# Kernel tuning notes

Hardware: AMD Instinct MI355X
Metric: run time of the kernel (lower is better)

Reference implementation:

```python
import jax, jax.numpy as jnp
import numpy as np

N = 100000
E = 1600000
IN_C = 128
HEADS = 4
HEAD_D = 32  # out_channels(128) // heads(4)


def setup_inputs() -> dict:
    key = jax.random.key(0)
    k1, k2, k3, k4, k5, k6 = jax.random.split(key, 6)
    x = jax.random.normal(k1, (N, IN_C), dtype=jnp.float32)
    edge_index = jax.random.randint(k2, (2, E), 0, N, dtype=jnp.int64)
    edge_weight = jax.random.uniform(k3, (E,), dtype=jnp.float32)
    # params: linear weight stored as [in, H*D] so forward is x @ W (torch does x @ weight.T)
    W = jax.random.normal(k4, (IN_C, HEADS * HEAD_D), dtype=jnp.float32) * (1.0 / np.sqrt(IN_C))
    att_src = jax.random.normal(k5, (HEADS, HEAD_D), dtype=jnp.float32) * 0.1
    att_dst = jax.random.normal(k6, (HEADS, HEAD_D), dtype=jnp.float32) * 0.1
    return {"x": x, "W": W, "att_src": att_src, "att_dst": att_dst,
            "edge_weight": edge_weight, "edge_index": edge_index, "num_nodes": N}


def reference(x, W, att_src, att_dst, edge_weight, edge_index, num_nodes):
    H, D = att_src.shape
    xw = (x @ W).reshape(-1, H, D)                       # [N, H, D]
    row, col = edge_index[0], edge_index[1]
    a_src = jnp.einsum('nhd,hd->nh', xw, att_src)        # [N, H]
    a_dst = jnp.einsum('nhd,hd->nh', xw, att_dst)        # [N, H]
    alpha = jax.nn.leaky_relu(a_src[row] + a_dst[col], negative_slope=0.2)  # [E, H]
    # segment softmax over edges grouped by row (destination of aggregation)
    amax = jax.ops.segment_max(alpha, row, num_segments=num_nodes)          # [N, H]
    amax = jnp.where(jnp.isfinite(amax), amax, 0.0)      # empty segments -> 0 (matches torch init)
    alpha = jnp.exp(alpha - amax[row])
    asum = jax.ops.segment_sum(alpha, row, num_segments=num_nodes)          # [N, H]
    alpha = alpha / (asum[row] + 1e-16)
    msg = xw[col] * alpha[..., None]                     # [E, H, D]
    out = jax.ops.segment_sum(msg, row, num_segments=num_nodes)             # [N, H, D]
    return out.reshape(num_nodes, H * D)
```

## Files before the change

kernel.cpp:

```cpp
#include <hip/hip_runtime.h>
#include <math.h>


typedef _Float16 half4 __attribute__((ext_vector_type(4)));
typedef _Float16 half8 __attribute__((ext_vector_type(8)));
typedef float    f32x4 __attribute__((ext_vector_type(4)));

#define PCHUNK   4096
#define NB_SHIFT 8
#define BCAP     4864

__device__ __forceinline__ float lrelu_exp(float v) {
    return __expf(fmaxf(v, 0.2f * v));
}

__global__ __launch_bounds__(128) void k_prep(const float* __restrict__ W,
                                              const float* __restrict__ att_src,
                                              const float* __restrict__ att_dst,
                                              _Float16* __restrict__ Wa) {
    int n = blockIdx.x;
    int k = threadIdx.x;
    float v;
    if (n < 128) {
        v = W[(size_t)k * 128 + n];
    } else if (n < 136) {
        int h = (n - 128) & 3;
        const float* att = (n < 132) ? att_src : att_dst;
        float s = 0.f;
        #pragma unroll
        for (int d = 0; d < 32; ++d)
            s += W[(size_t)k * 128 + h * 32 + d] * att[h * 32 + d];
        v = s;
    } else {
        v = 0.f;
    }
    Wa[n * 128 + k] = (_Float16)v;
}

__device__ __forceinline__ _Float16* lds_ptr(_Float16* base, int r, int kf16) {
    int g = (kf16 >> 3) ^ (r & 7);
    return base + r * 128 + g * 8 + (kf16 & 7);
}

__global__ __launch_bounds__(256) void k_gemm(const float* __restrict__ x,
                                              const _Float16* __restrict__ Wa,
                                              _Float16* __restrict__ xwh,
                                              float* __restrict__ a_src,
                                              float* __restrict__ a_dst, int N) {
    __shared__ _Float16 Xs[64 * 128];
    __shared__ _Float16 Ws[144 * 128];
    int t = threadIdx.x;
    int lane = t & 63, wv = t >> 6;
    int lm = lane & 15, lg = lane >> 4;
    int row0 = blockIdx.x * 64;

    #pragma unroll
    for (int i = 0; i < 9; ++i) {
        int f = (i * 256 + t) * 8;
        int nr = f >> 7, kc = f & 127;
        *(half8*)lds_ptr(Ws, nr, kc) = *(const half8*)&Wa[f];
    }
    #pragma unroll
    for (int i = 0; i < 4; ++i) {
        int f = (i * 256 + t) * 8;
        int r = f >> 7, kc = f & 127;
        int gr = row0 + r; if (gr >= N) gr = N - 1;
        float4 v0 = *(const float4*)&x[(size_t)gr * 128 + kc];
        float4 v1 = *(const float4*)&x[(size_t)gr * 128 + kc + 4];
        half8 hv;
        hv[0] = (_Float16)v0.x; hv[1] = (_Float16)v0.y;
        hv[2] = (_Float16)v0.z; hv[3] = (_Float16)v0.w;
        hv[4] = (_Float16)v1.x; hv[5] = (_Float16)v1.y;
        hv[6] = (_Float16)v1.z; hv[7] = (_Float16)v1.w;
        *(half8*)lds_ptr(Xs, r, kc) = hv;
    }
    __syncthreads();

    f32x4 acc[9];
    #pragma unroll
    for (int nn = 0; nn < 9; ++nn) acc[nn] = (f32x4){0.f, 0.f, 0.f, 0.f};

    #pragma unroll
    for (int kk = 0; kk < 4; ++kk) {
        int kb = kk * 32 + lg * 8;
        half8 a0 = *(const half8*)lds_ptr(Xs, wv * 16 + lm, kb);
        #pragma unroll
        for (int nn = 0; nn < 9; ++nn) {
            half8 b = *(const half8*)lds_ptr(Ws, nn * 16 + lm, kb);
            acc[nn] = __builtin_amdgcn_mfma_f32_16x16x32_f16(a0, b, acc[nn], 0, 0, 0);
        }
    }

    #pragma unroll
    for (int reg = 0; reg < 4; ++reg) {
        int row = row0 + wv * 16 + lg * 4 + reg;
        if (row < N) {
            #pragma unroll
            for (int nn = 0; nn < 8; ++nn)
                xwh[(size_t)row * 128 + nn * 16 + lm] = (_Float16)acc[nn][reg];
            float lv = acc[8][reg];
            if (lm < 4)      a_src[(size_t)row * 4 + lm]       = lv;
            else if (lm < 8) a_dst[(size_t)row * 4 + (lm - 4)] = lv;
        }
    }
}

__global__ __launch_bounds__(256) void k_part(const int* __restrict__ eidx,
                                              int* __restrict__ bctr,
                                              unsigned* __restrict__ rec,
                                              int E) {
    __shared__ unsigned long long buf[PCHUNK];
    __shared__ unsigned sbuf[PCHUNK];
    __shared__ int hist[512], excl[512], gbase[512], cur[512];
    __shared__ int wtot[4];
    int t = threadIdx.x;
    int lane = t & 63, wv = t >> 6;
    int e0 = blockIdx.x * PCHUNK;
    int nE = E - e0; if (nE > PCHUNK) nE = PCHUNK;
    hist[t] = 0; hist[t + 256] = 0;
    __syncthreads();
    for (int i = t; i < nE; i += 256) {
        int row = __builtin_nontemporal_load(&eidx[e0 + i]);
        int col = __builtin_nontemporal_load(&eidx[E + e0 + i]);
        buf[i] = ((unsigned long long)(unsigned)col << 32) | (unsigned)row;
        atomicAdd(&hist[row >> NB_SHIFT], 1);
    }
    __syncthreads();
    int h0 = hist[2 * t], h1 = hist[2 * t + 1];
    int s = h0 + h1, sc = s;
    #pragma unroll
    for (int off = 1; off < 64; off <<= 1) {
        int v = __shfl_up(sc, off);
        if (lane >= off) sc += v;
    }
    if (lane == 63) wtot[wv] = sc;
    __syncthreads();
    if (t == 0) {
        int run = 0;
        #pragma unroll
        for (int i = 0; i < 4; ++i) { int tmp = wtot[i]; wtot[i] = run; run += tmp; }
    }
    __syncthreads();
    int incl = sc + wtot[wv];
    excl[2 * t]     = incl - s;
    excl[2 * t + 1] = incl - h1;
    cur[2 * t]      = incl - s;
    cur[2 * t + 1]  = incl - h1;
    gbase[2 * t]     = h0 ? atomicAdd(&bctr[2 * t], h0) : 0;
    gbase[2 * t + 1] = h1 ? atomicAdd(&bctr[2 * t + 1], h1) : 0;
    __syncthreads();
    for (int i = t; i < nE; i += 256) {
        unsigned long long r = buf[i];
        int row = (int)(unsigned)r;
        int dst = atomicAdd(&cur[row >> NB_SHIFT], 1);
        sbuf[dst] = ((unsigned)(r >> 32) << 8) | ((unsigned)row & 255u);
    }
    __syncthreads();
    for (int j = t; j < nE; j += 256) {
        unsigned r = sbuf[j];
        int lo = 0;
        #pragma unroll
        for (int stp = 256; stp >= 1; stp >>= 1)
            if (lo + stp <= 511 && excl[lo + stp] <= j) lo += stp;
        int b = lo;
        int off = gbase[b] + (j - excl[b]);
        if (off < BCAP)
            __builtin_nontemporal_store(r, &rec[(size_t)b * BCAP + off]);
    }
}

__global__ __launch_bounds__(256) void k_csr(const unsigned* __restrict__ rec,
                                             const int* __restrict__ bctr,
                                             int2* __restrict__ rseg,
                                             int* __restrict__ csr_col, int N) {
    __shared__ int cnt[256], cur[256];
    __shared__ int wtot[4];
    int b = blockIdx.x;
    int rs = b << NB_SHIFT;
    int t = threadIdx.x;
    int lane = t & 63, wv = t >> 6;
    cnt[t] = 0;
    __syncthreads();
    int m = bctr[b]; if (m > BCAP) m = BCAP;
    const unsigned* rr = &rec[(size_t)b * BCAP];
    for (int i = t; i < m; i += 256) {
        unsigned r = rr[i];
        atomicAdd(&cnt[r & 255u], 1);
    }
    __syncthreads();
    int c = cnt[t], sc = c;
    #pragma unroll
    for (int off = 1; off < 64; off <<= 1) {
        int v = __shfl_up(sc, off);
        if (lane >= off) sc += v;
    }
    if (lane == 63) wtot[wv] = sc;
    __syncthreads();
    if (t == 0) {
        int run = 0;
        #pragma unroll
        for (int i = 0; i < 4; ++i) { int tmp = wtot[i]; wtot[i] = run; run += tmp; }
    }
    __syncthreads();
    int ex = sc + wtot[wv] - c;
    cur[t] = ex;
    int n = rs + t;
    if (n < N) {
        int2 sg;
        sg.x = b * BCAP + ex;
        sg.y = b * BCAP + ex + c;
        rseg[n] = sg;
    }
    __syncthreads();
    for (int i = t; i < m; i += 256) {
        unsigned r = rr[i];
        int slot = atomicAdd(&cur[r & 255u], 1);
        csr_col[b * BCAP + slot] = (int)(r >> 8);
    }
}

__global__ __launch_bounds__(256) void k_agg(const int2* __restrict__ rseg,
                                             const int* __restrict__ csr_col,
                                             const float* __restrict__ a_src,
                                             const float* __restrict__ a_dst,
                                             const _Float16* __restrict__ xwh,
                                             float* __restrict__ out, int N) {
    int lane = threadIdx.x & 63;
    int n = blockIdx.x * 4 + (threadIdx.x >> 6);
    if (n >= N) return;
    int2 seg = rseg[n];
    int beg = seg.x, end = seg.y;
    int q = lane >> 4;
    int l = lane & 15;
    int h = l >> 2;
    float s_n = a_src[(size_t)n * 4 + h];
    float acc[8] = {0, 0, 0, 0, 0, 0, 0, 0};
    float ws = 0.f;

    for (int w0 = beg; w0 < end; w0 += 64) {
        int rem = end - w0; if (rem > 64) rem = 64;
        int cc = (lane < rem) ? __builtin_nontemporal_load(&csr_col[w0 + lane]) : 0;
        int j = 0;
        for (; j + 16 <= rem; j += 16) {
            int c[4]; float ad[4]; half8 xv[4];
            #pragma unroll
            for (int u = 0; u < 4; ++u) c[u] = __shfl(cc, j + u * 4 + q);
            #pragma unroll
            for (int u = 0; u < 4; ++u) {
                ad[u] = a_dst[(size_t)c[u] * 4 + h];
                xv[u] = *(const half8*)&xwh[(size_t)c[u] * 128 + (l << 3)];
            }
            #pragma unroll
            for (int u = 0; u < 4; ++u) {
                float w = lrelu_exp(s_n + ad[u]);
                ws += w;
                #pragma unroll
                for (int k = 0; k < 8; ++k)
                    acc[k] += w * (float)xv[u][k];
            }
        }
        if (j < rem) {
            int c[4]; float m[4]; float ad[4]; half8 xv[4];
            #pragma unroll
            for (int u = 0; u < 4; ++u) {
                int r = j + u * 4 + q;
                c[u] = __shfl(cc, r);
                m[u] = (r < rem) ? 1.f : 0.f;
            }
            #pragma unroll
            for (int u = 0; u < 4; ++u) {
                ad[u] = a_dst[(size_t)c[u] * 4 + h];
                xv[u] = *(const half8*)&xwh[(size_t)c[u] * 128 + (l << 3)];
            }
            #pragma unroll
            for (int u = 0; u < 4; ++u) {
                float w = m[u] * lrelu_exp(s_n + ad[u]);
                ws += w;
                #pragma unroll
                for (int k = 0; k < 8; ++k)
                    acc[k] += w * (float)xv[u][k];
            }
        }
    }

    #pragma unroll
    for (int k = 0; k < 8; ++k) {
        acc[k] += __shfl_xor(acc[k], 16);
        acc[k] += __shfl_xor(acc[k], 32);
    }
    ws += __shfl_xor(ws, 16);
    ws += __shfl_xor(ws, 32);
    if (q == 0) {
        float inv = 1.0f / (ws + 1e-16f);
        f32x4 o0 = {acc[0] * inv, acc[1] * inv, acc[2] * inv, acc[3] * inv};
        f32x4 o1 = {acc[4] * inv, acc[5] * inv, acc[6] * inv, acc[7] * inv};
        __builtin_nontemporal_store(o0, (f32x4*)&out[(size_t)n * 128 + (l << 3)]);
        __builtin_nontemporal_store(o1, (f32x4*)&out[(size_t)n * 128 + (l << 3) + 4]);
    }
}

extern "C" void kernel_launch(void* const* d_in, const int* in_sizes, int n_in,
                              void* d_out, int out_size, void* d_ws, size_t ws_size,
                              hipStream_t stream) {
    const float* x       = (const float*)d_in[0];
    const float* W       = (const float*)d_in[1];
    const float* att_src = (const float*)d_in[2];
    const float* att_dst = (const float*)d_in[3];
    const int* eidx      = (const int*)d_in[5];
    int N = in_sizes[0] / 128;
    int E = in_sizes[4];
    float* out = (float*)d_out;

    char* p = (char*)d_ws;
    auto alloc = [&](size_t bytes) {
        char* r = p;
        p += (bytes + 255) & ~(size_t)255;
        return r;
    };
    int nbuckets = (N + 255) >> NB_SHIFT;
    _Float16* xwh  = (_Float16*)alloc((size_t)N * 128 * 2);
    float* a_src   = (float*)alloc((size_t)N * 4 * 4);
    float* a_dst   = (float*)alloc((size_t)N * 4 * 4);
    int*   bctr    = (int*)  alloc(512 * 4);
    unsigned* rec  = (unsigned*)alloc((size_t)nbuckets * BCAP * 4);
    int2*  rseg    = (int2*) alloc((size_t)N * 8);
    int*   csr_col = (int*)  alloc((size_t)nbuckets * BCAP * 4);
    _Float16* Wa   = (_Float16*)alloc(144 * 128 * 2);

    (void)hipMemsetAsync(bctr, 0, 512 * 4, stream);
    k_prep<<<144, 128, 0, stream>>>(W, att_src, att_dst, Wa);
    k_gemm<<<(N + 63) / 64, 256, 0, stream>>>(x, Wa, xwh, a_src, a_dst, N);
    k_part<<<(E + PCHUNK - 1) / PCHUNK, 256, 0, stream>>>(eidx, bctr, rec, E);
    k_csr<<<nbuckets, 256, 0, stream>>>(rec, bctr, rseg, csr_col, N);
    k_agg<<<(N + 3) / 4, 256, 0, stream>>>(rseg, csr_col, a_src, a_dst, xwh, out, N);
}
```

Before: 240.7 us.

## Record bucket ids during scatter and split aggregation into two launches

```diff
diff --git a/kernel.cpp b/kernel.cpp
--- a/kernel.cpp
+++ b/kernel.cpp
@@ -149,20 +149,30 @@
     gbase[2 * t]     = h0 ? atomicAdd(&bctr[2 * t], h0) : 0;
     gbase[2 * t + 1] = h1 ? atomicAdd(&bctr[2 * t + 1], h1) : 0;
     __syncthreads();
-    for (int i = t; i < nE; i += 256) {
-        unsigned long long r = buf[i];
-        int row = (int)(unsigned)r;
-        int dst = atomicAdd(&cur[row >> NB_SHIFT], 1);
-        sbuf[dst] = ((unsigned)(r >> 32) << 8) | ((unsigned)row & 255u);
+    unsigned long long myrec[PCHUNK / 256];
+    #pragma unroll
+    for (int k = 0; k < PCHUNK / 256; ++k) {
+        int i = t + k * 256;
+        if (i < nE) myrec[k] = buf[i];
+    }
+    __syncthreads();
+    unsigned short* bkt16 = (unsigned short*)buf;
+    #pragma unroll
+    for (int k = 0; k < PCHUNK / 256; ++k) {
+        int i = t + k * 256;
+        if (i < nE) {
+            unsigned long long r = myrec[k];
+            int row = (int)(unsigned)r;
+            int b = row >> NB_SHIFT;
+            int dst = atomicAdd(&cur[b], 1);
+            sbuf[dst] = ((unsigned)(r >> 32) << 8) | ((unsigned)row & 255u);
+            bkt16[dst] = (unsigned short)b;
+        }
     }
     __syncthreads();
     for (int j = t; j < nE; j += 256) {
         unsigned r = sbuf[j];
-        int lo = 0;
-        #pragma unroll
-        for (int stp = 256; stp >= 1; stp >>= 1)
-            if (lo + stp <= 511 && excl[lo + stp] <= j) lo += stp;
-        int b = lo;
+        int b = bkt16[j];
         int off = gbase[b] + (j - excl[b]);
         if (off < BCAP)
             __builtin_nontemporal_store(r, &rec[(size_t)b * BCAP + off]);
@@ -224,10 +234,11 @@
                                              const float* __restrict__ a_src,
                                              const float* __restrict__ a_dst,
                                              const _Float16* __restrict__ xwh,
-                                             float* __restrict__ out, int N) {
+                                             float* __restrict__ out,
+                                             int n0, int n1) {
     int lane = threadIdx.x & 63;
-    int n = blockIdx.x * 4 + (threadIdx.x >> 6);
-    if (n >= N) return;
+    int n = n0 + blockIdx.x * 4 + (threadIdx.x >> 6);
+    if (n >= n1) return;
     int2 seg = rseg[n];
     int beg = seg.x, end = seg.y;
     int q = lane >> 4;
@@ -332,5 +343,7 @@
     k_gemm<<<(N + 63) / 64, 256, 0, stream>>>(x, Wa, xwh, a_src, a_dst, N);
     k_part<<<(E + PCHUNK - 1) / PCHUNK, 256, 0, stream>>>(eidx, bctr, rec, E);
     k_csr<<<nbuckets, 256, 0, stream>>>(rec, bctr, rseg, csr_col, N);
-    k_agg<<<(N + 3) / 4, 256, 0, stream>>>(rseg, csr_col, a_src, a_dst, xwh, out, N);
-}
+    int half = N / 2;
+    k_agg<<<(half + 3) / 4, 256, 0, stream>>>(rseg, csr_col, a_src, a_dst, xwh, out, 0, half);
+    k_agg<<<(N - half + 3) / 4, 256, 0, stream>>>(rseg, csr_col, a_src, a_dst, xwh, out, half, N);
+}
```

New measurement: 240.1 us. No clear change (-0.3%).
